# Optimization experiments

Hardware: AMD Instinct MI355X
Metric: run time of the kernel (lower is better)

The kernel has to match this reference:

```python
import jax, jax.numpy as jnp
import numpy as np

N_SEND = 100000   # sender nodes
N_RECV = 100000   # receiver nodes
E = 600000        # edges
D = 128           # node feature channels (128x0e)
A = 8             # attr channels (8x0e)
S = 64            # edge scalar dim = fc_neurons[0]
H = 128           # fc hidden = fc_neurons[1]; tp.weight_numel = 128
NUM_NEIGHBORS = 32.0
SILU_NORM = 1.679177  # e3nn normalize2mom constant for silu: (E[silu(N(0,1))^2])^-0.5


def fctp(x, y, W):
    """e3nn FullyConnectedTensorProduct for all-scalar (0e) irreps:
    single 'uvw' path, path weight 1/sqrt(mul_u*mul_v)."""
    return jnp.einsum('nu,nv,uvw->nw', x, y, W) / np.sqrt(x.shape[1] * y.shape[1]).astype(np.float32)


def setup_inputs() -> dict:
    key = jax.random.key(0)
    ks = jax.random.split(key, 14)
    return {
        'sender_input': jax.random.normal(ks[0], (N_SEND, D), jnp.float32),
        'sender_attr': jax.random.normal(ks[1], (N_SEND, A), jnp.float32),
        'receiver_input': jax.random.normal(ks[2], (N_RECV, D), jnp.float32),
        'receiver_attr': jax.random.normal(ks[3], (N_RECV, A), jnp.float32),
        'edge_src': jax.random.randint(ks[4], (E,), 0, N_SEND, jnp.int32),
        'edge_dst': jax.random.randint(ks[5], (E,), 0, N_RECV, jnp.int32),
        'edge_attr': jax.random.normal(ks[6], (E, 1), jnp.float32),
        'edge_scalars': jax.random.normal(ks[7], (E, S), jnp.float32),
        # e3nn TP weights are initialized N(0,1)
        'W_sc': jax.random.normal(ks[8], (D, A, D), jnp.float32),
        'W_lin1': jax.random.normal(ks[9], (D, A, D), jnp.float32),
        'W_fc1': jax.random.normal(ks[10], (S, H), jnp.float32),
        'W_fc2': jax.random.normal(ks[11], (H, D), jnp.float32),
        'W_lin2': jax.random.normal(ks[12], (D, A, D), jnp.float32),
        'W_lin3': jax.random.normal(ks[13], (D, A, 1), jnp.float32),
    }


def reference(sender_input, sender_attr, receiver_input, receiver_attr,
              edge_src, edge_dst, edge_attr, edge_scalars,
              W_sc, W_lin1, W_fc1, W_fc2, W_lin2, W_lin3):
    # FullyConnectedNet([S, H, weight_numel], silu): act(x@W/sqrt(fan_in)), last layer linear
    h = SILU_NORM * jax.nn.silu(edge_scalars @ W_fc1 / np.sqrt(S).astype(np.float32))
    weight = h @ W_fc2 / np.sqrt(H).astype(np.float32)                     # [E, D] per-edge TP weights

    receiver_self_connection = fctp(receiver_input, receiver_attr, W_sc)   # [Nr, D]
    sender_features = fctp(sender_input, sender_attr, W_lin1)              # [Ns, D]

    # gather -> per-edge weighted ('uvu') tensor product with 1x0e edge_attr -> scatter-add
    edge_features = weight * sender_features[edge_src] * edge_attr         # [E, D]
    receiver_features = jax.ops.segment_sum(edge_features, edge_dst,
                                            num_segments=receiver_input.shape[0])
    receiver_features = receiver_features / np.sqrt(NUM_NEIGHBORS).astype(np.float32)

    receiver_conv_out = fctp(receiver_features, receiver_attr, W_lin2)     # [Nr, D]
    receiver_angle = 0.1 * fctp(receiver_features, receiver_attr, W_lin3)  # [Nr, 1]
    # sc.output_mask is all-ones for this irreps config, so sin gating applies to all channels
    return jnp.cos(receiver_angle) * receiver_self_connection + jnp.sin(receiver_angle) * receiver_conv_out
```

## Files before the change

kernel.cpp:

```cpp
#include <hip/hip_runtime.h>
#include <hip/hip_bf16.h>
#include <math.h>

#define NS 100000
#define NR 100000
#define NE 600000
#define SILU_NORM 1.679177f

typedef __attribute__((ext_vector_type(8))) short short8;
typedef __attribute__((ext_vector_type(4))) float f32x4;

static __device__ __forceinline__ short f2bf(float f) {
    return __builtin_bit_cast(short, __float2bfloat16(f));
}

#define GLDS16(g, l)                                                         \
    __builtin_amdgcn_global_load_lds(                                        \
        (const __attribute__((address_space(1))) unsigned int*)(const void*)(g), \
        (__attribute__((address_space(3))) unsigned int*)(void*)(l), 16, 0, 0)

__global__ void swz_kernel(const float* __restrict__ W,
                           __hip_bfloat16* __restrict__ out, int total)
{
    int idx = blockIdx.x * 256 + threadIdx.x;
    if (idx >= total) return;
    int s = idx >> 12, r = idx & 4095;
    int f = r >> 9;  r &= 511;
    int quad = r >> 7; r &= 127;
    int wl = r >> 3;
    int j = r & 7;
    int k = s * 32 + quad * 8 + j;
    int w = f * 16 + wl;
    out[idx] = __float2bfloat16(W[(size_t)k * 128 + w]);
}

__global__ __launch_bounds__(256) void fctp_mfma_kernel(
    const float* __restrict__ x, const float* __restrict__ y,
    const __hip_bfloat16* __restrict__ Wswz, float* __restrict__ out,
    float scale, int N)
{
    __shared__ __hip_bfloat16 Wb[8192];
    __shared__ float xs[128 * 8];

    const int tid = threadIdx.x;
    const int lane = tid & 63;
    const int wv = tid >> 6;
    const int quad = lane >> 4;
    const int wl = lane & 15;
    const int n0 = blockIdx.x * 128;

    float ya[2][8];
    #pragma unroll
    for (int mt = 0; mt < 2; ++mt) {
        int node = n0 + wv * 32 + mt * 16 + wl;
        if (node >= N) node = N - 1;
        const float4* yp = (const float4*)(y + (size_t)node * 8);
        float4 a = yp[0], b = yp[1];
        ya[mt][0] = a.x; ya[mt][1] = a.y; ya[mt][2] = a.z; ya[mt][3] = a.w;
        ya[mt][4] = b.x; ya[mt][5] = b.y; ya[mt][6] = b.z; ya[mt][7] = b.w;
    }

    f32x4 acc[2][8];
    #pragma unroll
    for (int mt = 0; mt < 2; ++mt)
        #pragma unroll
        for (int f = 0; f < 8; ++f)
            acc[mt][f] = (f32x4){0.f, 0.f, 0.f, 0.f};

    for (int cc = 0; cc < 16; ++cc) {
        __syncthreads();
        {
            const char* src = (const char*)(Wswz + (size_t)cc * 8192);
            #pragma unroll
            for (int i = 0; i < 4; ++i) {
                int off = (i * 256 + tid) * 16;
                GLDS16(src + off, (char*)Wb + off);
            }
            int nl = tid >> 1, c4 = (tid & 1) * 4;
            int node = n0 + nl;
            if (node >= N) node = N - 1;
            GLDS16(x + (size_t)node * 128 + cc * 8 + c4, (char*)xs + tid * 16);
        }
        __syncthreads();

        #pragma unroll
        for (int ks = 0; ks < 2; ++ks) {
            short8 bfr[8];
            #pragma unroll
            for (int f = 0; f < 8; ++f)
                bfr[f] = *(const short8*)((const short*)Wb +
                                          (size_t)ks * 4096 + (f * 64 + lane) * 8);
            #pragma unroll
            for (int mt = 0; mt < 2; ++mt) {
                float xv = xs[(wv * 32 + mt * 16 + wl) * 8 + ks * 4 + quad];
                short8 af;
                #pragma unroll
                for (int v = 0; v < 8; ++v) af[v] = f2bf(xv * ya[mt][v]);
                #pragma unroll
                for (int f = 0; f < 8; ++f)
                    acc[mt][f] = __builtin_amdgcn_mfma_f32_16x16x32_bf16(
                        af, bfr[f], acc[mt][f], 0, 0, 0);
            }
        }
    }

    #pragma unroll
    for (int mt = 0; mt < 2; ++mt) {
        #pragma unroll
        for (int r = 0; r < 4; ++r) {
            int node = n0 + wv * 32 + mt * 16 + quad * 4 + r;
            if (node < N) {
                #pragma unroll
                for (int f = 0; f < 8; ++f)
                    out[(size_t)node * 128 + f * 16 + wl] = acc[mt][f][r] * scale;
            }
        }
    }
}

__global__ __launch_bounds__(256, 4) void edge_mfma_kernel(
    const int* __restrict__ esrc, const int* __restrict__ edst,
    const float* __restrict__ eattr, const float* __restrict__ escal,
    const __hip_bfloat16* __restrict__ W1swz,
    const __hip_bfloat16* __restrict__ W2swz,
    const float* __restrict__ sf, float* __restrict__ rfeat)
{
    __shared__ __hip_bfloat16 hA[16384];

    const int tid = threadIdx.x;
    const int lane = tid & 63;
    const int wv = tid >> 6;
    const int quad = lane >> 4;
    const int wl = lane & 15;
    const int e0 = blockIdx.x * 128;

    short8 af1[2][2];
    #pragma unroll
    for (int ks = 0; ks < 2; ++ks)
        #pragma unroll
        for (int mt = 0; mt < 2; ++mt) {
            int e = e0 + (wv * 2 + mt) * 16 + wl;
            if (e >= NE) e = NE - 1;
            const float4* p = (const float4*)(escal + (size_t)e * 64 + ks * 32 + quad * 8);
            float4 a = p[0], b = p[1];
            short8 v;
            v[0] = f2bf(a.x); v[1] = f2bf(a.y); v[2] = f2bf(a.z); v[3] = f2bf(a.w);
            v[4] = f2bf(b.x); v[5] = f2bf(b.y); v[6] = f2bf(b.z); v[7] = f2bf(b.w);
            af1[ks][mt] = v;
        }

    f32x4 acc1[2][8];
    #pragma unroll
    for (int mt = 0; mt < 2; ++mt)
        #pragma unroll
        for (int f = 0; f < 8; ++f) acc1[mt][f] = (f32x4){0.f, 0.f, 0.f, 0.f};

    #pragma unroll
    for (int ks = 0; ks < 2; ++ks)
        #pragma unroll
        for (int f = 0; f < 8; ++f) {
            short8 bfr = *(const short8*)((const short*)W1swz +
                                          (size_t)ks * 4096 + (f * 64 + lane) * 8);
            acc1[0][f] = __builtin_amdgcn_mfma_f32_16x16x32_bf16(
                af1[ks][0], bfr, acc1[0][f], 0, 0, 0);
            acc1[1][f] = __builtin_amdgcn_mfma_f32_16x16x32_bf16(
                af1[ks][1], bfr, acc1[1][f], 0, 0, 0);
        }

    #pragma unroll
    for (int mt = 0; mt < 2; ++mt) {
        int MT = wv * 2 + mt;
        #pragma unroll
        for (int f = 0; f < 8; ++f) {
            int s2 = f >> 1;
            int q2 = ((f & 1) * 2 + (wl >> 3)) & 3;
            int j2 = wl & 7;
            #pragma unroll
            for (int r = 0; r < 4; ++r) {
                float t = acc1[mt][f][r] * 0.125f;
                float h = SILU_NORM * t / (1.f + __expf(-t));
                int lpos = q2 * 16 + quad * 4 + r;
                ((short*)hA)[((size_t)(s2 * 8 + MT) * 64 + lpos) * 8 + j2] = f2bf(h);
            }
        }
    }
    __syncthreads();

    f32x4 acc2[2][8];
    #pragma unroll
    for (int mt = 0; mt < 2; ++mt)
        #pragma unroll
        for (int f = 0; f < 8; ++f) acc2[mt][f] = (f32x4){0.f, 0.f, 0.f, 0.f};

    #pragma unroll
    for (int ks = 0; ks < 4; ++ks) {
        short8 afA = *(const short8*)((const short*)hA +
                                      ((size_t)(ks * 8 + wv * 2 + 0) * 64 + lane) * 8);
        short8 afB = *(const short8*)((const short*)hA +
                                      ((size_t)(ks * 8 + wv * 2 + 1) * 64 + lane) * 8);
        #pragma unroll
        for (int f = 0; f < 8; ++f) {
            short8 bfr = *(const short8*)((const short*)W2swz +
                                          (size_t)ks * 4096 + (f * 64 + lane) * 8);
            acc2[0][f] = __builtin_amdgcn_mfma_f32_16x16x32_bf16(
                afA, bfr, acc2[0][f], 0, 0, 0);
            acc2[1][f] = __builtin_amdgcn_mfma_f32_16x16x32_bf16(
                afB, bfr, acc2[1][f], 0, 0, 0);
        }
    }

    const float s128 = 0.08838834764831845f;
    #pragma unroll
    for (int mt = 0; mt < 2; ++mt) {
        int MT = wv * 2 + mt;
        #pragma unroll
        for (int r = 0; r < 4; ++r) {
            int e = e0 + MT * 16 + quad * 4 + r;
            if (e < NE) {
                int src = esrc[e], dst = edst[e];
                float ea = eattr[e] * s128;
                #pragma unroll
                for (int f = 0; f < 8; ++f) {
                    float val = acc2[mt][f][r] * ea *
                                sf[(size_t)src * 128 + f * 16 + wl];
                    atomicAdd(&rfeat[(size_t)dst * 128 + f * 16 + wl], val);
                }
            }
        }
    }
}

__global__ __launch_bounds__(256) void conv_fuse_kernel(
    const float* __restrict__ x, const float* __restrict__ y,
    const __hip_bfloat16* __restrict__ Wswz, const float* __restrict__ W3,
    const float* __restrict__ rsc, float* __restrict__ out, int N)
{
    __shared__ __hip_bfloat16 Wb[8192];
    __shared__ float xs[128 * 8];

    const int tid = threadIdx.x;
    const int lane = tid & 63;
    const int wv = tid >> 6;
    const int quad = lane >> 4;
    const int wl = lane & 15;
    const int n0 = blockIdx.x * 128;

    float ya[2][8];
    #pragma unroll
    for (int mt = 0; mt < 2; ++mt) {
        int node = n0 + wv * 32 + mt * 16 + wl;
        if (node >= N) node = N - 1;
        const float4* yp = (const float4*)(y + (size_t)node * 8);
        float4 a = yp[0], b = yp[1];
        ya[mt][0] = a.x; ya[mt][1] = a.y; ya[mt][2] = a.z; ya[mt][3] = a.w;
        ya[mt][4] = b.x; ya[mt][5] = b.y; ya[mt][6] = b.z; ya[mt][7] = b.w;
    }

    f32x4 acc[2][8];
    #pragma unroll
    for (int mt = 0; mt < 2; ++mt)
        #pragma unroll
        for (int f = 0; f < 8; ++f)
            acc[mt][f] = (f32x4){0.f, 0.f, 0.f, 0.f};
    float aacc[2] = {0.f, 0.f};

    for (int cc = 0; cc < 16; ++cc) {
        __syncthreads();
        {
            const char* src = (const char*)(Wswz + (size_t)cc * 8192);
            #pragma unroll
            for (int i = 0; i < 4; ++i) {
                int off = (i * 256 + tid) * 16;
                GLDS16(src + off, (char*)Wb + off);
            }
            int nl = tid >> 1, c4 = (tid & 1) * 4;
            int node = n0 + nl;
            if (node >= N) node = N - 1;
            GLDS16(x + (size_t)node * 128 + cc * 8 + c4, (char*)xs + tid * 16);
        }
        __syncthreads();

        #pragma unroll
        for (int ks = 0; ks < 2; ++ks) {
            short8 bfr[8];
            #pragma unroll
            for (int f = 0; f < 8; ++f)
                bfr[f] = *(const short8*)((const short*)Wb +
                                          (size_t)ks * 4096 + (f * 64 + lane) * 8);
            const float4* wp = (const float4*)(W3 + ((cc * 8 + ks * 4 + quad) * 8));
            float4 w3a = wp[0], w3b = wp[1];
            float w3v[8] = {w3a.x, w3a.y, w3a.z, w3a.w, w3b.x, w3b.y, w3b.z, w3b.w};
            #pragma unroll
            for (int mt = 0; mt < 2; ++mt) {
                float xv = xs[(wv * 32 + mt * 16 + wl) * 8 + ks * 4 + quad];
                short8 af;
                #pragma unroll
                for (int v = 0; v < 8; ++v) {
                    float p = xv * ya[mt][v];
                    af[v] = f2bf(p);
                    aacc[mt] += p * w3v[v];
                }
                #pragma unroll
                for (int f = 0; f < 8; ++f)
                    acc[mt][f] = __builtin_amdgcn_mfma_f32_16x16x32_bf16(
                        af, bfr[f], acc[mt][f], 0, 0, 0);
            }
        }
    }

    float ared[2];
    #pragma unroll
    for (int mt = 0; mt < 2; ++mt) {
        float a = aacc[mt];
        a += __shfl_xor(a, 16);
        a += __shfl_xor(a, 32);
        ared[mt] = a * 5.524271728019903e-4f;
    }

    const float cs = 5.524271728019903e-3f;
    #pragma unroll
    for (int mt = 0; mt < 2; ++mt) {
        #pragma unroll
        for (int r = 0; r < 4; ++r) {
            int node = n0 + wv * 32 + mt * 16 + quad * 4 + r;
            float a = __shfl(ared[mt], quad * 4 + r);
            if (node < N) {
                float ca = __cosf(a), sa = __sinf(a);
                #pragma unroll
                for (int f = 0; f < 8; ++f) {
                    size_t o = (size_t)node * 128 + f * 16 + wl;
                    out[o] = ca * rsc[o] + sa * (acc[mt][f][r] * cs);
                }
            }
        }
    }
}

extern "C" void kernel_launch(void* const* d_in, const int* in_sizes, int n_in,
                              void* d_out, int out_size, void* d_ws, size_t ws_size,
                              hipStream_t stream)
{
    const float* sender_input   = (const float*)d_in[0];
    const float* sender_attr    = (const float*)d_in[1];
    const float* receiver_input = (const float*)d_in[2];
    const float* receiver_attr  = (const float*)d_in[3];
    const int*   edge_src  = (const int*)d_in[4];
    const int*   edge_dst  = (const int*)d_in[5];
    const float* edge_attr = (const float*)d_in[6];
    const float* edge_scal = (const float*)d_in[7];
    const float* W_sc   = (const float*)d_in[8];
    const float* W_lin1 = (const float*)d_in[9];
    const float* W_fc1  = (const float*)d_in[10];
    const float* W_fc2  = (const float*)d_in[11];
    const float* W_lin2 = (const float*)d_in[12];
    const float* W_lin3 = (const float*)d_in[13];

    char* ws = (char*)d_ws;
    float* sf    = (float*)(ws);
    float* rfeat = (float*)(ws + 51200000);
    __hip_bfloat16* Wl1s = (__hip_bfloat16*)(ws + 102400000);
    __hip_bfloat16* Wscs = (__hip_bfloat16*)(ws + 102662144);
    __hip_bfloat16* Wl2s = (__hip_bfloat16*)(ws + 102924288);
    __hip_bfloat16* W1s  = (__hip_bfloat16*)(ws + 103186432);
    __hip_bfloat16* W2s  = (__hip_bfloat16*)(ws + 103202816);
    float* rsc = sf;

    swz_kernel<<<512, 256, 0, stream>>>(W_lin1, Wl1s, 131072);
    swz_kernel<<<512, 256, 0, stream>>>(W_sc,   Wscs, 131072);
    swz_kernel<<<512, 256, 0, stream>>>(W_lin2, Wl2s, 131072);
    swz_kernel<<<32,  256, 0, stream>>>(W_fc1,  W1s,  8192);
    swz_kernel<<<64,  256, 0, stream>>>(W_fc2,  W2s,  16384);

    hipMemsetAsync(rfeat, 0, (size_t)NR * 128 * 4, stream);

    fctp_mfma_kernel<<<(NS + 127) / 128, 256, 0, stream>>>(
        sender_input, sender_attr, Wl1s, sf, 0.03125f, NS);
    edge_mfma_kernel<<<(NE + 127) / 128, 256, 0, stream>>>(
        edge_src, edge_dst, edge_attr, edge_scal, W1s, W2s, sf, rfeat);
    fctp_mfma_kernel<<<(NR + 127) / 128, 256, 0, stream>>>(
        receiver_input, receiver_attr, Wscs, rsc, 0.03125f, NR);
    conv_fuse_kernel<<<(NR + 127) / 128, 256, 0, stream>>>(
        rfeat, receiver_attr, Wl2s, W_lin3, rsc, (float*)d_out, NR);
}
```

Baseline: 747.7 us.

## Sort edges by destination and combine runs before atomics; double-buffer FCTP staging

Builds a counting-sort permutation of edges by destination using a histogram, a three-pass scan and an atomic scatter. The edge kernel processes edges in that order and sums consecutive same-destination rows in registers before issuing atomicAdds. Both FCTP kernels get double-buffered LDS staging so the next chunk loads while the current one computes. It also adds a duplicated first-layer MFMA pass whose results are zeroed and thrown away. Gathers of edge_scalars become random, several small kernels are added, and d_out is borrowed as scratch space.

After: 698.3 us. 1.07x faster.

```diff
diff --git a/kernel.cpp b/kernel.cpp
--- a/kernel.cpp
+++ b/kernel.cpp
@@ -34,13 +34,97 @@
     out[idx] = __float2bfloat16(W[(size_t)k * 128 + w]);
 }
 
+__global__ __launch_bounds__(256) void hist_kernel(const int* __restrict__ edst,
+                                                   int* __restrict__ cnt)
+{
+    int i = blockIdx.x * 256 + threadIdx.x;
+    if (i < NE) atomicAdd(&cnt[edst[i]], 1);
+}
+
+#define SCAN_BLK 1024
+
+__global__ __launch_bounds__(256) void scan1_kernel(const int* __restrict__ cnt,
+                                                    int* __restrict__ bsum, int n)
+{
+    __shared__ int ts[256];
+    int b = blockIdx.x, t = threadIdx.x;
+    int base = b * SCAN_BLK + t * 4;
+    int s = 0;
+    #pragma unroll
+    for (int k = 0; k < 4; ++k) { int i = base + k; if (i < n) s += cnt[i]; }
+    ts[t] = s; __syncthreads();
+    #pragma unroll
+    for (int off = 128; off; off >>= 1) {
+        if (t < off) ts[t] += ts[t + off];
+        __syncthreads();
+    }
+    if (t == 0) bsum[b] = ts[0];
+}
+
+__global__ __launch_bounds__(128) void scan2_kernel(const int* __restrict__ bsum,
+                                                    int* __restrict__ bofs, int nb)
+{
+    __shared__ int sh[128];
+    int t = threadIdx.x;
+    sh[t] = (t < nb) ? bsum[t] : 0;
+    __syncthreads();
+    for (int off = 1; off < 128; off <<= 1) {
+        int v = (t >= off) ? sh[t - off] : 0;
+        __syncthreads();
+        sh[t] += v;
+        __syncthreads();
+    }
+    if (t < nb) bofs[t] = (t == 0) ? 0 : sh[t - 1];
+}
+
+__global__ __launch_bounds__(256) void scan3_kernel(const int* __restrict__ cnt,
+                                                    const int* __restrict__ bofs,
+                                                    int* __restrict__ ofs, int n)
+{
+    __shared__ int ts[256];
+    int b = blockIdx.x, t = threadIdx.x;
+    int base = b * SCAN_BLK + t * 4;
+    int v[4]; int s = 0;
+    #pragma unroll
+    for (int k = 0; k < 4; ++k) {
+        int i = base + k;
+        v[k] = (i < n) ? cnt[i] : 0;
+        s += v[k];
+    }
+    ts[t] = s; __syncthreads();
+    for (int off = 1; off < 256; off <<= 1) {
+        int u = (t >= off) ? ts[t - off] : 0;
+        __syncthreads();
+        ts[t] += u;
+        __syncthreads();
+    }
+    int run = bofs[b] + ts[t] - s;
+    #pragma unroll
+    for (int k = 0; k < 4; ++k) {
+        int i = base + k;
+        if (i < n) ofs[i] = run;
+        run += v[k];
+    }
+}
+
+__global__ __launch_bounds__(256) void scatter_kernel(const int* __restrict__ edst,
+                                                      int* __restrict__ ofs,
+                                                      int* __restrict__ perm)
+{
+    int i = blockIdx.x * 256 + threadIdx.x;
+    if (i < NE) {
+        int pos = atomicAdd(&ofs[edst[i]], 1);
+        perm[pos] = i;
+    }
+}
+
 __global__ __launch_bounds__(256) void fctp_mfma_kernel(
     const float* __restrict__ x, const float* __restrict__ y,
     const __hip_bfloat16* __restrict__ Wswz, float* __restrict__ out,
     float scale, int N)
 {
-    __shared__ __hip_bfloat16 Wb[8192];
-    __shared__ float xs[128 * 8];
+    __shared__ __hip_bfloat16 Wb[2][8192];
+    __shared__ float xs[2][128 * 8];
 
     const int tid = threadIdx.x;
     const int lane = tid & 63;
@@ -67,32 +151,36 @@
         for (int f = 0; f < 8; ++f)
             acc[mt][f] = (f32x4){0.f, 0.f, 0.f, 0.f};
 
+    auto stage = [&](int b, int cc) {
+        const char* src = (const char*)(Wswz + (size_t)cc * 8192);
+        #pragma unroll
+        for (int i = 0; i < 4; ++i) {
+            int off = (i * 256 + tid) * 16;
+            GLDS16(src + off, (char*)Wb[b] + off);
+        }
+        int nl = tid >> 1, c4 = (tid & 1) * 4;
+        int node = n0 + nl;
+        if (node >= N) node = N - 1;
+        GLDS16(x + (size_t)node * 128 + cc * 8 + c4, (char*)xs[b] + tid * 16);
+    };
+
+    stage(0, 0);
+    __syncthreads();
+
     for (int cc = 0; cc < 16; ++cc) {
-        __syncthreads();
-        {
-            const char* src = (const char*)(Wswz + (size_t)cc * 8192);
-            #pragma unroll
-            for (int i = 0; i < 4; ++i) {
-                int off = (i * 256 + tid) * 16;
-                GLDS16(src + off, (char*)Wb + off);
-            }
-            int nl = tid >> 1, c4 = (tid & 1) * 4;
-            int node = n0 + nl;
-            if (node >= N) node = N - 1;
-            GLDS16(x + (size_t)node * 128 + cc * 8 + c4, (char*)xs + tid * 16);
-        }
-        __syncthreads();
+        int cur = cc & 1;
+        if (cc < 15) stage(cur ^ 1, cc + 1);
 
         #pragma unroll
         for (int ks = 0; ks < 2; ++ks) {
             short8 bfr[8];
             #pragma unroll
             for (int f = 0; f < 8; ++f)
-                bfr[f] = *(const short8*)((const short*)Wb +
+                bfr[f] = *(const short8*)((const short*)Wb[cur] +
                                           (size_t)ks * 4096 + (f * 64 + lane) * 8);
             #pragma unroll
             for (int mt = 0; mt < 2; ++mt) {
-                float xv = xs[(wv * 32 + mt * 16 + wl) * 8 + ks * 4 + quad];
+                float xv = xs[cur][(wv * 32 + mt * 16 + wl) * 8 + ks * 4 + quad];
                 short8 af;
                 #pragma unroll
                 for (int v = 0; v < 8; ++v) af[v] = f2bf(xv * ya[mt][v]);
@@ -102,6 +190,7 @@
                         af, bfr[f], acc[mt][f], 0, 0, 0);
             }
         }
+        __syncthreads();
     }
 
     #pragma unroll
@@ -121,6 +210,7 @@
 __global__ __launch_bounds__(256, 4) void edge_mfma_kernel(
     const int* __restrict__ esrc, const int* __restrict__ edst,
     const float* __restrict__ eattr, const float* __restrict__ escal,
+    const int* __restrict__ perm,
     const __hip_bfloat16* __restrict__ W1swz,
     const __hip_bfloat16* __restrict__ W2swz,
     const float* __restrict__ sf, float* __restrict__ rfeat)
@@ -134,14 +224,21 @@
     const int wl = lane & 15;
     const int e0 = blockIdx.x * 128;
 
+    int epm[2];
+    #pragma unroll
+    for (int mt = 0; mt < 2; ++mt) {
+        int j = e0 + (wv * 2 + mt) * 16 + wl;
+        if (j >= NE) j = NE - 1;
+        epm[mt] = perm[j];
+    }
+
     short8 af1[2][2];
     #pragma unroll
     for (int ks = 0; ks < 2; ++ks)
         #pragma unroll
         for (int mt = 0; mt < 2; ++mt) {
-            int e = e0 + (wv * 2 + mt) * 16 + wl;
-            if (e >= NE) e = NE - 1;
-            const float4* p = (const float4*)(escal + (size_t)e * 64 + ks * 32 + quad * 8);
+            const float4* p = (const float4*)(escal + (size_t)epm[mt] * 64 +
+                                              ks * 32 + quad * 8);
             float4 a = p[0], b = p[1];
             short8 v;
             v[0] = f2bf(a.x); v[1] = f2bf(a.y); v[2] = f2bf(a.z); v[3] = f2bf(a.w);
@@ -155,6 +252,22 @@
         #pragma unroll
         for (int f = 0; f < 8; ++f) acc1[mt][f] = (f32x4){0.f, 0.f, 0.f, 0.f};
 
+    #pragma unroll
+    for (int ks = 0; ks < 2; ++ks)
+        #pragma unroll
+        for (int f = 0; f < 8; ++f) {
+            short8 bfr = *(const short8*)((const short*)W1swz +
+                                          (size_t)ks * 4096 + (f * 64 + lane) * 8);
+            acc1[0][f] = __builtin_amdgcn_mfma_f32_16x16x32_bf16(
+                af1[0][0], bfr, acc1[0][f], 0, 0, 0);
+            acc1[1][f] = __builtin_amdgcn_mfma_f32_16x16x32_bf16(
+                af1[0][1], bfr, acc1[1][f], 0, 0, 0);
+        }
+
+    #pragma unroll
+    for (int mt = 0; mt < 2; ++mt)
+        #pragma unroll
+        for (int f = 0; f < 8; ++f) acc1[mt][f] = (f32x4){0.f, 0.f, 0.f, 0.f};
     #pragma unroll
     for (int ks = 0; ks < 2; ++ks)
         #pragma unroll
@@ -212,20 +325,46 @@
     const float s128 = 0.08838834764831845f;
     #pragma unroll
     for (int mt = 0; mt < 2; ++mt) {
-        int MT = wv * 2 + mt;
-        #pragma unroll
-        for (int r = 0; r < 4; ++r) {
-            int e = e0 + MT * 16 + quad * 4 + r;
-            if (e < NE) {
-                int src = esrc[e], dst = edst[e];
-                float ea = eattr[e] * s128;
-                #pragma unroll
-                for (int f = 0; f < 8; ++f) {
-                    float val = acc2[mt][f][r] * ea *
-                                sf[(size_t)src * 128 + f * 16 + wl];
-                    atomicAdd(&rfeat[(size_t)dst * 128 + f * 16 + wl], val);
+        int jbase = e0 + (wv * 2 + mt) * 16 + quad * 4;
+        if (jbase < NE) {
+            int4 pj = *(const int4*)(perm + jbase);
+            int dsts[4], srcs[4];
+            float eas[4];
+            #pragma unroll
+            for (int r = 0; r < 4; ++r) {
+                int e = (r == 0) ? pj.x : (r == 1) ? pj.y : (r == 2) ? pj.z : pj.w;
+                dsts[r] = edst[e];
+                srcs[r] = esrc[e];
+                eas[r]  = eattr[e] * s128;
+            }
+            float run[8];
+            int curdst = dsts[0];
+            #pragma unroll
+            for (int f = 0; f < 8; ++f)
+                run[f] = acc2[mt][f][0] * eas[0] *
+                         sf[(size_t)srcs[0] * 128 + f * 16 + wl];
+            #pragma unroll
+            for (int r = 1; r < 4; ++r) {
+                float val[8];
+                #pragma unroll
+                for (int f = 0; f < 8; ++f)
+                    val[f] = acc2[mt][f][r] * eas[r] *
+                             sf[(size_t)srcs[r] * 128 + f * 16 + wl];
+                if (dsts[r] == curdst) {
+                    #pragma unroll
+                    for (int f = 0; f < 8; ++f) run[f] += val[f];
+                } else {
+                    #pragma unroll
+                    for (int f = 0; f < 8; ++f)
+                        atomicAdd(&rfeat[(size_t)curdst * 128 + f * 16 + wl], run[f]);
+                    curdst = dsts[r];
+                    #pragma unroll
+                    for (int f = 0; f < 8; ++f) run[f] = val[f];
                 }
             }
+            #pragma unroll
+            for (int f = 0; f < 8; ++f)
+                atomicAdd(&rfeat[(size_t)curdst * 128 + f * 16 + wl], run[f]);
         }
     }
 }
@@ -235,8 +374,8 @@
     const __hip_bfloat16* __restrict__ Wswz, const float* __restrict__ W3,
     const float* __restrict__ rsc, float* __restrict__ out, int N)
 {
-    __shared__ __hip_bfloat16 Wb[8192];
-    __shared__ float xs[128 * 8];
+    __shared__ __hip_bfloat16 Wb[2][8192];
+    __shared__ float xs[2][128 * 8];
 
     const int tid = threadIdx.x;
     const int lane = tid & 63;
@@ -264,41 +403,45 @@
             acc[mt][f] = (f32x4){0.f, 0.f, 0.f, 0.f};
     float aacc[2] = {0.f, 0.f};
 
+    auto stage = [&](int b, int cc) {
+        const char* src = (const char*)(Wswz + (size_t)cc * 8192);
+        #pragma unroll
+        for (int i = 0; i < 4; ++i) {
+            int off = (i * 256 + tid) * 16;
+            GLDS16(src + off, (char*)Wb[b] + off);
+        }
+        int nl = tid >> 1, c4 = (tid & 1) * 4;
+        int node = n0 + nl;
+        if (node >= N) node = N - 1;
+        GLDS16(x + (size_t)node * 128 + cc * 8 + c4, (char*)xs[b] + tid * 16);
+    };
+
+    stage(0, 0);
+    __syncthreads();
+
     for (int cc = 0; cc < 16; ++cc) {
-        __syncthreads();
-        {
-            const char* src = (const char*)(Wswz + (size_t)cc * 8192);
-            #pragma unroll
-            for (int i = 0; i < 4; ++i) {
-                int off = (i * 256 + tid) * 16;
-                GLDS16(src + off, (char*)Wb + off);
-            }
-            int nl = tid >> 1, c4 = (tid & 1) * 4;
-            int node = n0 + nl;
-            if (node >= N) node = N - 1;
-            GLDS16(x + (size_t)node * 128 + cc * 8 + c4, (char*)xs + tid * 16);
-        }
-        __syncthreads();
+        int cur = cc & 1;
+        if (cc < 15) stage(cur ^ 1, cc + 1);
 
         #pragma unroll
         for (int ks = 0; ks < 2; ++ks) {
             short8 bfr[8];
             #pragma unroll
             for (int f = 0; f < 8; ++f)
-                bfr[f] = *(const short8*)((const short*)Wb +
+                bfr[f] = *(const short8*)((const short*)Wb[cur] +
                                           (size_t)ks * 4096 + (f * 64 + lane) * 8);
             const float4* wp = (const float4*)(W3 + ((cc * 8 + ks * 4 + quad) * 8));
             float4 w3a = wp[0], w3b = wp[1];
             float w3v[8] = {w3a.x, w3a.y, w3a.z, w3a.w, w3b.x, w3b.y, w3b.z, w3b.w};
             #pragma unroll
             for (int mt = 0; mt < 2; ++mt) {
-                float xv = xs[(wv * 32 + mt * 16 + wl) * 8 + ks * 4 + quad];
+                float xv = xs[cur][(wv * 32 + mt * 16 + wl) * 8 + ks * 4 + quad];
                 short8 af;
                 #pragma unroll
                 for (int v = 0; v < 8; ++v) {
-                    float p = xv * ya[mt][v];
-                    af[v] = f2bf(p);
-                    aacc[mt] += p * w3v[v];
+                    float pr = xv * ya[mt][v];
+                    af[v] = f2bf(pr);
+                    aacc[mt] += pr * w3v[v];
                 }
                 #pragma unroll
                 for (int f = 0; f < 8; ++f)
@@ -306,6 +449,7 @@
                         af, bfr[f], acc[mt][f], 0, 0, 0);
             }
         }
+        __syncthreads();
     }
 
     float ared[2];
@@ -365,6 +509,12 @@
     __hip_bfloat16* W2s  = (__hip_bfloat16*)(ws + 103202816);
     float* rsc = sf;
 
+    int* perm = (int*)d_out;
+    int* cnt  = (int*)d_out + 600000;
+    int* ofs  = (int*)d_out + 700000;
+    int* bsum = (int*)d_out + 800000;
+    int* bofs = (int*)d_out + 800128;
+
     swz_kernel<<<512, 256, 0, stream>>>(W_lin1, Wl1s, 131072);
     swz_kernel<<<512, 256, 0, stream>>>(W_sc,   Wscs, 131072);
     swz_kernel<<<512, 256, 0, stream>>>(W_lin2, Wl2s, 131072);
@@ -372,11 +522,19 @@
     swz_kernel<<<64,  256, 0, stream>>>(W_fc2,  W2s,  16384);
 
     hipMemsetAsync(rfeat, 0, (size_t)NR * 128 * 4, stream);
+    hipMemsetAsync(cnt, 0, (size_t)NR * 4, stream);
+
+    const int nbScan = (NR + SCAN_BLK - 1) / SCAN_BLK;
+    hist_kernel<<<(NE + 255) / 256, 256, 0, stream>>>(edge_dst, cnt);
+    scan1_kernel<<<nbScan, 256, 0, stream>>>(cnt, bsum, NR);
+    scan2_kernel<<<1, 128, 0, stream>>>(bsum, bofs, nbScan);
+    scan3_kernel<<<nbScan, 256, 0, stream>>>(cnt, bofs, ofs, NR);
+    scatter_kernel<<<(NE + 255) / 256, 256, 0, stream>>>(edge_dst, ofs, perm);
 
     fctp_mfma_kernel<<<(NS + 127) / 128, 256, 0, stream>>>(
         sender_input, sender_attr, Wl1s, sf, 0.03125f, NS);
     edge_mfma_kernel<<<(NE + 127) / 128, 256, 0, stream>>>(
-        edge_src, edge_dst, edge_attr, edge_scal, W1s, W2s, sf, rfeat);
+        edge_src, edge_dst, edge_attr, edge_scal, perm, W1s, W2s, sf, rfeat);
     fctp_mfma_kernel<<<(NR + 127) / 128, 256, 0, stream>>>(
         receiver_input, receiver_attr, Wscs, rsc, 0.03125f, NR);
     conv_fuse_kernel<<<(NR + 127) / 128, 256, 0, stream>>>(
```
